# Optimization experiments

Hardware: AMD Instinct MI355X
Metric: run time of the kernel (lower is better)

The kernel has to match this reference:

```python
import jax, jax.numpy as jnp
import numpy as np

G, NPG = 100, 500
N = G * NPG            # 50000 nodes, contiguous equal-size graphs
IN, H = 128, 256
L = 3                  # num_layers
K = 3                  # knn k (loop=True -> self included)
E = 16 * N             # 800000 edges

def setup_inputs():
    key = jax.random.key(0)
    k = jax.random.split(key, 8)
    x = jax.random.normal(k[0], (N, IN), jnp.float32)
    batch = jnp.repeat(jnp.arange(G, dtype=jnp.int32), NPG)
    gid = jax.random.randint(k[1], (E,), 0, G)
    src = jax.random.randint(k[2], (E,), 0, NPG) + gid * NPG
    dst = jax.random.randint(k[3], (E,), 0, NPG) + gid * NPG
    edge_index = jnp.stack([src, dst]).astype(jnp.int32)
    def lin(kk, fin, fout):
        return (jax.random.normal(kk, (fin, fout), jnp.float32) / np.sqrt(fin)).astype(jnp.float32)
    inp = dict(x=x, edge_index=edge_index, batch=batch)
    inp["emb_W"] = lin(k[4], IN, H); inp["emb_b"] = jnp.zeros((H,), jnp.float32)
    inp["conv_W"] = jnp.stack([lin(jax.random.fold_in(k[5], i), H, H) for i in range(L)])
    inp["conv_b"] = jnp.zeros((L, H), jnp.float32)
    inp["fconv_W"] = jnp.stack([lin(jax.random.fold_in(k[6], i), H, H) for i in range(L)])
    inp["fconv_b"] = jnp.zeros((L, H), jnp.float32)
    inp["norm_w"] = jnp.ones((L, H), jnp.float32); inp["norm_b"] = jnp.zeros((L, H), jnp.float32); inp["norm_ms"] = jnp.ones((L, H), jnp.float32)
    inp["fnorm_w"] = jnp.ones((L, H), jnp.float32); inp["fnorm_b"] = jnp.zeros((L, H), jnp.float32); inp["fnorm_ms"] = jnp.ones((L, H), jnp.float32)
    inp["gate_W"] = lin(k[7], 2 * H, H); inp["gate_b"] = jnp.zeros((H,), jnp.float32)
    return inp

def _gcn_conv(h, src, dst, W, b):
    # GCNConv: add self loops, symmetric deg^-1/2 normalization
    m = h @ W                                     # [N,H]
    loop = jnp.arange(N, dtype=src.dtype)
    s2 = jnp.concatenate([src, loop]); d2 = jnp.concatenate([dst, loop])
    deg = jax.ops.segment_sum(jnp.ones_like(d2, jnp.float32), d2, num_segments=N)
    dinv = jnp.where(deg > 0, jax.lax.rsqrt(deg), 0.0)
    coef = (dinv[s2] * dinv[d2])[:, None]
    return jax.ops.segment_sum(m[s2] * coef, d2, num_segments=N) + b

def _graph_norm(x, batch, w, b, ms, cnt):
    # PyG GraphNorm: out = w * (x - ms*mean) / sqrt(var + eps) + b, per-graph stats
    mean = jax.ops.segment_sum(x, batch, num_segments=G) / cnt
    out = x - mean[batch] * ms
    var = jax.ops.segment_sum(out * out, batch, num_segments=G) / cnt
    return w * out * jax.lax.rsqrt(var + 1e-5)[batch] + b

def _knn_graph(x):
    # per-graph cosine knn, loop=True (self has sim 1 and is kept)
    xr = x.reshape(G, NPG, -1)
    xn = xr / (jnp.linalg.norm(xr, axis=-1, keepdims=True) + 1e-12)
    sim = jnp.einsum('gnh,gmh->gnm', xn, xn)      # [G,NPG,NPG]
    _, idx = jax.lax.top_k(sim, K)                # [G,NPG,K]
    offs = (jnp.arange(G) * NPG)[:, None, None]
    src = (idx + offs).reshape(-1)
    dst = jnp.broadcast_to(jnp.arange(N).reshape(G, NPG, 1), (G, NPG, K)).reshape(-1)
    return src.astype(jnp.int32), dst.astype(jnp.int32)

def reference(x, edge_index, batch, emb_W, emb_b, conv_W, conv_b, norm_w, norm_b, norm_ms, fconv_W, fconv_b, fnorm_w, fnorm_b, fnorm_ms, gate_W, gate_b):
    cnt = jax.ops.segment_sum(jnp.ones((N,), jnp.float32), batch, num_segments=G)[:, None]
    h = x @ emb_W + emb_b
    fsrc, fdst = _knn_graph(h)
    src, dst = edge_index[0], edge_index[1]
    all_x = []
    for i in range(L - 1):   # eval mode: dropout is identity
        prev = h
        h = _gcn_conv(h, src, dst, conv_W[i], conv_b[i])
        h = jax.nn.leaky_relu(_graph_norm(h, batch, norm_w[i], norm_b[i], norm_ms[i], cnt))
        f = _gcn_conv(h, fsrc, fdst, fconv_W[i], fconv_b[i])
        f = jax.nn.leaky_relu(_graph_norm(f, batch, fnorm_w[i], fnorm_b[i], fnorm_ms[i], cnt))
        gate = jax.nn.sigmoid(jnp.concatenate([h, f], axis=-1) @ gate_W + gate_b)
        h = gate * h + (1.0 - gate) * f + prev
        all_x.append(h)
    # faithful to source: for i in range(L): += pool(all_x[i-1])  (Python negative indexing!)
    gf = jnp.zeros((G, H), jnp.float32)
    for i in range(L):
        gf = gf + jax.ops.segment_sum(all_x[i - 1], batch, num_segments=G) / cnt
    return gf
```

## Files before the change

kernel.cpp:

```cpp
#include <hip/hip_runtime.h>
#include <math.h>

#define NN 50000
#define GG 100
#define NPGc 500
#define HH 256
#define IND 128

typedef __attribute__((ext_vector_type(8))) short short8v;
typedef __attribute__((ext_vector_type(4))) float f32x4;

__device__ __forceinline__ ushort f2bf(float f) {
    union { float f; unsigned u; } v; v.f = f;
    unsigned r = (v.u + 0x7fffu + ((v.u >> 16) & 1u)) >> 16;
    return (ushort)r;
}
__device__ __forceinline__ float bf2f(ushort h) {
    union { unsigned u; float f; } v; v.u = ((unsigned)h) << 16;
    return v.f;
}

__device__ __forceinline__ int swz(int row, int kidx) { return kidx ^ ((row & 7) << 3); }

__global__ void wcvt(const float* __restrict__ src, ushort* __restrict__ dst, int K, int N)
{
    int i = blockIdx.x * 256 + threadIdx.x;
    if (i < K * N) {
        int n = i / K, k = i % K;
        dst[i] = f2bf(src[(size_t)k * N + n]);
    }
}

__global__ __launch_bounds__(256)
void gemm_mfma(const float* __restrict__ A, const float* __restrict__ A2,
               const ushort* __restrict__ Wt, const float* __restrict__ bias,
               float* __restrict__ C, ushort* __restrict__ Cbf,
               int M, int K, int lda, int mode,
               const float* __restrict__ hn, const float* __restrict__ fn,
               const float* __restrict__ prev)
{
    __shared__ ushort As[128][64];
    __shared__ ushort Bs[128][64];
    const int tid = threadIdx.x;
    const int lane = tid & 63;
    const int w = tid >> 6;
    const int wr = (w >> 1) * 64, wc = (w & 1) * 64;
    const int row0 = blockIdx.x * 128, col0 = blockIdx.y * 128;
    const int lr = lane & 15, lk = (lane >> 4) * 8;
    f32x4 acc[4][4] = {};

    for (int k0 = 0; k0 < K; k0 += 64) {
        __syncthreads();
        #pragma unroll
        for (int it = 0; it < 4; ++it) {
            int c = it * 256 + tid;
            int row = c >> 3, col = (c & 7) * 8;
            int gr = row0 + row; if (gr > M - 1) gr = M - 1;
            const float* Ap = A; int kk = k0 + col;
            if (A2 != nullptr && kk >= 256) { Ap = A2; kk -= 256; }
            const float* s = &Ap[(size_t)gr * lda + kk];
            float4 v0 = *(const float4*)s;
            float4 v1 = *(const float4*)(s + 4);
            union { ushort u[8]; int4 q; } pk;
            pk.u[0] = f2bf(v0.x); pk.u[1] = f2bf(v0.y); pk.u[2] = f2bf(v0.z); pk.u[3] = f2bf(v0.w);
            pk.u[4] = f2bf(v1.x); pk.u[5] = f2bf(v1.y); pk.u[6] = f2bf(v1.z); pk.u[7] = f2bf(v1.w);
            *(int4*)&As[row][swz(row, col)] = pk.q;
        }
        #pragma unroll
        for (int it = 0; it < 4; ++it) {
            int c = it * 256 + tid;
            int n = c >> 3, k = (c & 7) * 8;
            *(int4*)&Bs[n][swz(n, k)] = *(const int4*)&Wt[(size_t)(col0 + n) * K + k0 + k];
        }
        __syncthreads();
        #pragma unroll
        for (int ks = 0; ks < 2; ++ks) {
            short8v av[4], bv[4];
            #pragma unroll
            for (int m = 0; m < 4; ++m) {
                int rr = wr + m * 16 + lr;
                av[m] = *(const short8v*)&As[rr][swz(rr, ks * 32 + lk)];
            }
            #pragma unroll
            for (int n = 0; n < 4; ++n) {
                int rr = wc + n * 16 + lr;
                bv[n] = *(const short8v*)&Bs[rr][swz(rr, ks * 32 + lk)];
            }
            #pragma unroll
            for (int m = 0; m < 4; ++m)
                #pragma unroll
                for (int n = 0; n < 4; ++n)
                    acc[m][n] = __builtin_amdgcn_mfma_f32_16x16x32_bf16(av[m], bv[n], acc[m][n], 0, 0, 0);
        }
    }
    const int fr = (lane >> 4) * 4;
    if (mode == 0) {
        #pragma unroll
        for (int n = 0; n < 4; ++n) {
            int col = col0 + wc + n * 16 + lr;
            float bb = bias ? bias[col] : 0.f;
            #pragma unroll
            for (int m = 0; m < 4; ++m) {
                int rbase = row0 + wr + m * 16 + fr;
                #pragma unroll
                for (int r = 0; r < 4; ++r) {
                    int row = rbase + r;
                    if (row < M) C[(size_t)row * HH + col] = acc[m][n][r] + bb;
                }
            }
        }
    } else if (mode == 2) {
        #pragma unroll
        for (int n = 0; n < 4; ++n) {
            int col = col0 + wc + n * 16 + lr;
            float bb = bias ? bias[col] : 0.f;
            #pragma unroll
            for (int m = 0; m < 4; ++m) {
                int rbase = row0 + wr + m * 16 + fr;
                #pragma unroll
                for (int r = 0; r < 4; ++r) {
                    int row = rbase + r;
                    if (row < M) Cbf[(size_t)row * HH + col] = f2bf(acc[m][n][r] + bb);
                }
            }
        }
    } else {
        #pragma unroll
        for (int n = 0; n < 4; ++n) {
            int col = col0 + wc + n * 16 + lr;
            float gb = bias[col];
            #pragma unroll
            for (int m = 0; m < 4; ++m) {
                int rbase = row0 + wr + m * 16 + fr;
                #pragma unroll
                for (int r = 0; r < 4; ++r) {
                    int row = rbase + r;
                    if (row < M) {
                        size_t o = (size_t)row * HH + col;
                        float z = acc[m][n][r] + gb;
                        float s = 1.f / (1.f + expf(-z));
                        C[o] = s * hn[o] + (1.f - s) * fn[o] + prev[o];
                    }
                }
            }
        }
    }
}

__global__ __launch_bounds__(256)
void row_norm_hl(const float* __restrict__ h, ushort* __restrict__ xh, ushort* __restrict__ xl)
{
    int n = blockIdx.x, c = threadIdx.x;
    float v = h[(size_t)n * HH + c];
    __shared__ float red[256];
    red[c] = v * v;
    __syncthreads();
    for (int s = 128; s > 0; s >>= 1) {
        if (c < s) red[c] += red[c + s];
        __syncthreads();
    }
    float norm = sqrtf(red[0]);
    float xn = v / (norm + 1e-12f);
    ushort hi = f2bf(xn);
    xh[(size_t)n * HH + c] = hi;
    xl[(size_t)n * HH + c] = f2bf(xn - bf2f(hi));
}

__device__ __forceinline__ bool tk_better(float va, int ia, float vb, int ib)
{
    return (va > vb) || (va == vb && ia < ib);
}

__device__ __forceinline__ void ins3(float v, int i,
                                     float& a0, int& b0, float& a1, int& b1,
                                     float& a2, int& b2)
{
    if (tk_better(v, i, a0, b0))      { a2 = a1; b2 = b1; a1 = a0; b1 = b0; a0 = v; b0 = i; }
    else if (tk_better(v, i, a1, b1)) { a2 = a1; b2 = b1; a1 = v;  b1 = i; }
    else if (tk_better(v, i, a2, b2)) { a2 = v;  b2 = i; }
}

__device__ __forceinline__ void merge3(float& v0, float& v1, float& v2,
                                       int& i0, int& i1, int& i2, int off)
{
    float w0 = __shfl_xor(v0, off), w1 = __shfl_xor(v1, off), w2 = __shfl_xor(v2, off);
    int   j0 = __shfl_xor(i0, off), j1 = __shfl_xor(i1, off), j2 = __shfl_xor(i2, off);
    float avv[3] = { v0, v1, v2 }, bvv[3] = { w0, w1, w2 };
    int   aii[3] = { i0, i1, i2 }, bii[3] = { j0, j1, j2 };
    float rv[3]; int ri[3];
    int p = 0, q = 0;
    #pragma unroll
    for (int t = 0; t < 3; ++t) {
        bool takeA = tk_better(avv[p], aii[p], bvv[q], bii[q]);
        rv[t] = takeA ? avv[p] : bvv[q];
        ri[t] = takeA ? aii[p] : bii[q];
        if (takeA) ++p; else ++q;
    }
    v0 = rv[0]; v1 = rv[1]; v2 = rv[2];
    i0 = ri[0]; i1 = ri[1]; i2 = ri[2];
}

__global__ __launch_bounds__(256, 2)
void simtopk(const ushort* __restrict__ xnh, const ushort* __restrict__ xnl,
             int* __restrict__ fsrc)
{
    __shared__ ushort Ash[64][64], Asl[64][64];
    __shared__ ushort Bsh[128][64], Bsl[128][64];
    const int bid = blockIdx.x;
    const int xcd = bid & 7;
    const int rb  = (bid >> 3) & 7;
    const int g   = (bid >> 6) * 8 + xcd;
    if (g >= GG) return;
    const int row0 = rb * 64;
    const int tid  = threadIdx.x;
    const int lane = tid & 63;
    const int w    = tid >> 6;
    const int lr   = lane & 15;
    const int hi4  = lane >> 4;
    const int lk   = hi4 * 8;
    const size_t base = (size_t)g * NPGc * HH;

    float tv0[4], tv1[4], tv2[4];
    int   ti0[4], ti1[4], ti2[4];
    #pragma unroll
    for (int r = 0; r < 4; ++r) {
        tv0[r] = tv1[r] = tv2[r] = -2.f;
        ti0[r] = ti1[r] = ti2[r] = 0x7fffffff;
    }

    for (int ct = 0; ct < 4; ++ct) {
        const int col0 = ct * 128;
        f32x4 acc[8] = {};
        for (int k0 = 0; k0 < HH; k0 += 64) {
            __syncthreads();
            #pragma unroll
            for (int it = 0; it < 2; ++it) {
                int flat = it * 256 + tid;
                int row = flat >> 3, col = (flat & 7) * 8;
                int grow = row0 + row; if (grow > NPGc - 1) grow = NPGc - 1;
                size_t o = base + (size_t)grow * HH + k0 + col;
                *(int4*)&Ash[row][swz(row, col)] = *(const int4*)(xnh + o);
                *(int4*)&Asl[row][swz(row, col)] = *(const int4*)(xnl + o);
            }
            #pragma unroll
            for (int it = 0; it < 4; ++it) {
                int flat = it * 256 + tid;
                int row = flat >> 3, col = (flat & 7) * 8;
                int gcol = col0 + row; if (gcol > NPGc - 1) gcol = NPGc - 1;
                size_t o = base + (size_t)gcol * HH + k0 + col;
                *(int4*)&Bsh[row][swz(row, col)] = *(const int4*)(xnh + o);
                *(int4*)&Bsl[row][swz(row, col)] = *(const int4*)(xnl + o);
            }
            __syncthreads();
            #pragma unroll
            for (int ks = 0; ks < 2; ++ks) {
                const int ra = w * 16 + lr;
                short8v ah = *(const short8v*)&Ash[ra][swz(ra, ks * 32 + lk)];
                short8v al = *(const short8v*)&Asl[ra][swz(ra, ks * 32 + lk)];
                #pragma unroll
                for (int n = 0; n < 8; ++n) {
                    const int rbn = n * 16 + lr;
                    short8v bh = *(const short8v*)&Bsh[rbn][swz(rbn, ks * 32 + lk)];
                    short8v bl = *(const short8v*)&Bsl[rbn][swz(rbn, ks * 32 + lk)];
                    acc[n] = __builtin_amdgcn_mfma_f32_16x16x32_bf16(ah, bh, acc[n], 0, 0, 0);
                    acc[n] = __builtin_amdgcn_mfma_f32_16x16x32_bf16(ah, bl, acc[n], 0, 0, 0);
                    acc[n] = __builtin_amdgcn_mfma_f32_16x16x32_bf16(al, bh, acc[n], 0, 0, 0);
                }
            }
        }
        #pragma unroll
        for (int r = 0; r < 4; ++r) {
            float a0 = tv0[r], a1 = tv1[r], a2 = tv2[r];
            int   b0 = ti0[r], b1 = ti1[r], b2 = ti2[r];
            #pragma unroll
            for (int n = 0; n < 8; ++n) {
                int col = col0 + n * 16 + lr;
                if (col < NPGc)
                    ins3(acc[n][r], col, a0, b0, a1, b1, a2, b2);
            }
            tv0[r] = a0; tv1[r] = a1; tv2[r] = a2;
            ti0[r] = b0; ti1[r] = b1; ti2[r] = b2;
        }
    }

    #pragma unroll
    for (int r = 0; r < 4; ++r) {
        float a0 = tv0[r], a1 = tv1[r], a2 = tv2[r];
        int   b0 = ti0[r], b1 = ti1[r], b2 = ti2[r];
        #pragma unroll
        for (int off = 1; off <= 8; off <<= 1)
            merge3(a0, a1, a2, b0, b1, b2, off);
        if (lr == 0) {
            int row = row0 + w * 16 + hi4 * 4 + r;
            if (row < NPGc) {
                int rg = g * NPGc + row;
                fsrc[rg * 3 + 0] = g * NPGc + b0;
                fsrc[rg * 3 + 1] = g * NPGc + b1;
                fsrc[rg * 3 + 2] = g * NPGc + b2;
            }
        }
    }
}

__global__ void hist_kernel(const int* __restrict__ dst, int* __restrict__ cnt, int nE)
{
    int e = blockIdx.x * 256 + threadIdx.x;
    if (e < nE) atomicAdd(&cnt[dst[e]], 1);
}

__global__ void scan1_kernel(const int* __restrict__ in, int* __restrict__ out,
                             int* __restrict__ bsum, int n)
{
    __shared__ int sh[256];
    int t = threadIdx.x;
    int i = blockIdx.x * 256 + t;
    int v = (i < n) ? in[i] : 0;
    sh[t] = v;
    __syncthreads();
    for (int s = 1; s < 256; s <<= 1) {
        int tv = (t >= s) ? sh[t - s] : 0;
        __syncthreads();
        sh[t] += tv;
        __syncthreads();
    }
    if (i < n) out[i] = sh[t] - v;
    if (t == 255) bsum[blockIdx.x] = sh[255];
}

__global__ void scan2_kernel(int* __restrict__ bsum, int nb)
{
    __shared__ int sh[256];
    int t = threadIdx.x;
    int v = (t < nb) ? bsum[t] : 0;
    sh[t] = v;
    __syncthreads();
    for (int s = 1; s < 256; s <<= 1) {
        int tv = (t >= s) ? sh[t - s] : 0;
        __syncthreads();
        sh[t] += tv;
        __syncthreads();
    }
    if (t < nb) bsum[t] = sh[t] - v;
}

__global__ void scan3_kernel(int* __restrict__ out, const int* __restrict__ bsum, int n)
{
    int i = blockIdx.x * 256 + threadIdx.x;
    if (i < n) out[i] += bsum[blockIdx.x];
}

__global__ void fill_kernel(const int* __restrict__ src, const int* __restrict__ dst,
                            const int* __restrict__ row_ptr, int* __restrict__ cursor,
                            int* __restrict__ sorted_src, int nE)
{
    int e = blockIdx.x * 256 + threadIdx.x;
    if (e < nE) {
        int d = dst[e];
        int pos = row_ptr[d] + atomicAdd(&cursor[d], 1);
        sorted_src[pos] = src[e];
    }
}

__global__ void dinv_kernel(const int* __restrict__ cnt, float* __restrict__ dinv, int n)
{
    int i = blockIdx.x * 256 + threadIdx.x;
    if (i < n) dinv[i] = rsqrtf((float)cnt[i] + 1.0f);
}

__global__ __launch_bounds__(256)
void gcn_gather(const ushort* __restrict__ m, const int* __restrict__ row_ptr,
                const int* __restrict__ cnt, const int* __restrict__ srcs,
                const float* __restrict__ dinv, const float* __restrict__ bias,
                float* __restrict__ out)
{
    int bid = blockIdx.x;
    int xcd = bid & 7, idx = bid >> 3;
    int g = xcd + 8 * (idx / NPGc);
    if (g >= GG) return;
    int n = g * NPGc + (idx % NPGc);
    int c = threadIdx.x;
    float dn = dinv[n];
    float acc = bf2f(m[(size_t)n * HH + c]) * dn;
    int s0 = row_ptr[n], e0 = s0 + cnt[n];
    for (int e = s0; e < e0; ++e) {
        int s = srcs[e];
        acc += bf2f(m[(size_t)s * HH + c]) * dinv[s];
    }
    out[(size_t)n * HH + c] = acc * dn + bias[c];
}

__global__ __launch_bounds__(256)
void fgcn_gather(const ushort* __restrict__ m, const int* __restrict__ fsrc,
                 const float* __restrict__ bias, float* __restrict__ out)
{
    int bid = blockIdx.x;
    int xcd = bid & 7, idx = bid >> 3;
    int g = xcd + 8 * (idx / NPGc);
    if (g >= GG) return;
    int n = g * NPGc + (idx % NPGc);
    int c = threadIdx.x;
    int s0 = fsrc[n * 3], s1 = fsrc[n * 3 + 1], s2 = fsrc[n * 3 + 2];
    float acc = bf2f(m[(size_t)n * HH + c]) + bf2f(m[(size_t)s0 * HH + c])
              + bf2f(m[(size_t)s1 * HH + c]) + bf2f(m[(size_t)s2 * HH + c]);
    out[(size_t)n * HH + c] = 0.25f * acc + bias[c];
}

__global__ __launch_bounds__(256)
void norm_stats(const float* __restrict__ x, float* __restrict__ S1, float* __restrict__ S2)
{
    int g = blockIdx.x, chunk = blockIdx.y, c = threadIdx.x;
    int r0 = chunk * 63, r1 = min(r0 + 63, NPGc);
    float s1 = 0.f, s2 = 0.f;
    for (int r = r0; r < r1; ++r) {
        float v = x[((size_t)(g * NPGc + r)) * HH + c];
        s1 += v; s2 += v * v;
    }
    atomicAdd(&S1[g * HH + c], s1);
    atomicAdd(&S2[g * HH + c], s2);
}

__global__ __launch_bounds__(256)
void norm_apply(float* __restrict__ x, const float* __restrict__ S1, const float* __restrict__ S2,
                const float* __restrict__ w, const float* __restrict__ b,
                const float* __restrict__ ms)
{
    int n = blockIdx.x, c = threadIdx.x;
    int g = n / NPGc;
    size_t o = (size_t)n * HH + c;
    float v = x[o];
    float mean = S1[g * HH + c] / (float)NPGc;
    float mm = mean * ms[c];
    float var = S2[g * HH + c] / (float)NPGc - 2.f * mm * mean + mm * mm;
    float outv = w[c] * (v - mm) * rsqrtf(var + 1e-5f) + b[c];
    x[o] = outv > 0.f ? outv : 0.01f * outv;
}

__global__ __launch_bounds__(256)
void pool_kernel(const float* __restrict__ X0, const float* __restrict__ X1,
                 float* __restrict__ out)
{
    int g = blockIdx.x, c = threadIdx.x;
    float s0 = 0.f, s1 = 0.f;
    for (int r = 0; r < NPGc; ++r) {
        size_t o = ((size_t)(g * NPGc + r)) * HH + c;
        s0 += X0[o];
        s1 += X1[o];
    }
    out[g * HH + c] = (s0 + 2.f * s1) / (float)NPGc;
}

__global__ void sentinel_kernel(float* out, int n)
{
    int i = blockIdx.x * 256 + threadIdx.x;
    if (i < n) out[i] = 12345.0f;
}

extern "C" void kernel_launch(void* const* d_in, const int* in_sizes, int n_in,
                              void* d_out, int out_size, void* d_ws, size_t ws_size,
                              hipStream_t stream)
{
    const float* x       = (const float*)d_in[0];
    const int* edge_idx  = (const int*)d_in[1];
    const float* emb_W   = (const float*)d_in[3];
    const float* emb_b   = (const float*)d_in[4];
    const float* conv_W  = (const float*)d_in[5];
    const float* conv_b  = (const float*)d_in[6];
    const float* fconv_W = (const float*)d_in[7];
    const float* fconv_b = (const float*)d_in[8];
    const float* norm_w  = (const float*)d_in[9];
    const float* norm_b  = (const float*)d_in[10];
    const float* norm_ms = (const float*)d_in[11];
    const float* fnorm_w = (const float*)d_in[12];
    const float* fnorm_b = (const float*)d_in[13];
    const float* fnorm_ms= (const float*)d_in[14];
    const float* gate_W  = (const float*)d_in[15];
    const float* gate_b  = (const float*)d_in[16];

    const int E = in_sizes[1] / 2;
    const int* esrc = edge_idx;
    const int* edst = edge_idx + E;

    const size_t NHf = (size_t)NN * HH;
    char* p = (char*)d_ws;
    auto alloc = [&](size_t bytes) { char* r = p; p += (bytes + 255) & ~(size_t)255; return r; };
    float* B0 = (float*)alloc(NHf * 4);
    float* B1 = (float*)alloc(NHf * 4);
    float* B2 = (float*)alloc(NHf * 4);
    float* B3 = (float*)alloc(NHf * 4);
    ushort* xnh = (ushort*)B2;
    ushort* xnl = xnh + NHf;
    ushort* msgbf = (ushort*)alloc(NHf * 2);
    int* sorted_src = (int*)alloc((size_t)E * 4);
    int* row_ptr    = (int*)alloc((size_t)NN * 4);
    int* deg_cnt    = (int*)alloc((size_t)NN * 4);
    int* cursor     = (int*)alloc((size_t)NN * 4);
    float* dinv     = (float*)alloc((size_t)NN * 4);
    int* fsrc       = (int*)alloc((size_t)NN * 3 * 4);
    float* S1       = (float*)alloc((size_t)GG * HH * 4);
    float* S2       = (float*)alloc((size_t)GG * HH * 4);
    int* bsum       = (int*)alloc(1024);
    ushort* wts     = (ushort*)alloc((size_t)425984 * 2);
    size_t needed = (size_t)(p - (char*)d_ws);
    if (ws_size < needed) {
        sentinel_kernel<<<(out_size + 255) / 256, 256, 0, stream>>>((float*)d_out, out_size);
        return;
    }
    ushort* embWt   = wts;
    ushort* convWt0 = wts + 32768;
    ushort* convWt1 = wts + 32768 + 65536;
    ushort* fconvWt0 = wts + 163840;
    ushort* fconvWt1 = wts + 163840 + 65536;
    ushort* gateWt  = wts + 294912;

    const int nScanB = (NN + 255) / 256;
    const int gatherGrid = 8 * 13 * NPGc;

    hipMemsetAsync(deg_cnt, 0, (size_t)NN * 4, stream);
    hipMemsetAsync(cursor, 0, (size_t)NN * 4, stream);

    wcvt<<<(32768 + 255) / 256, 256, 0, stream>>>(emb_W, embWt, IND, HH);
    wcvt<<<(65536 + 255) / 256, 256, 0, stream>>>(conv_W, convWt0, HH, HH);
    wcvt<<<(65536 + 255) / 256, 256, 0, stream>>>(conv_W + 65536, convWt1, HH, HH);
    wcvt<<<(65536 + 255) / 256, 256, 0, stream>>>(fconv_W, fconvWt0, HH, HH);
    wcvt<<<(65536 + 255) / 256, 256, 0, stream>>>(fconv_W + 65536, fconvWt1, HH, HH);
    wcvt<<<(131072 + 255) / 256, 256, 0, stream>>>(gate_W, gateWt, 2 * HH, HH);

    dim3 ggrid((NN + 127) / 128, 2);
    gemm_mfma<<<ggrid, 256, 0, stream>>>(x, nullptr, embWt, emb_b, B0, nullptr,
                                         NN, IND, IND, 0, nullptr, nullptr, nullptr);

    hist_kernel<<<(E + 255) / 256, 256, 0, stream>>>(edst, deg_cnt, E);
    scan1_kernel<<<nScanB, 256, 0, stream>>>(deg_cnt, row_ptr, bsum, NN);
    scan2_kernel<<<1, 256, 0, stream>>>(bsum, nScanB);
    scan3_kernel<<<nScanB, 256, 0, stream>>>(row_ptr, bsum, NN);
    fill_kernel<<<(E + 255) / 256, 256, 0, stream>>>(esrc, edst, row_ptr, cursor, sorted_src, E);
    dinv_kernel<<<(NN + 255) / 256, 256, 0, stream>>>(deg_cnt, dinv, NN);

    row_norm_hl<<<NN, 256, 0, stream>>>(B0, xnh, xnl);
    simtopk<<<832, 256, 0, stream>>>(xnh, xnl, fsrc);

    float* h  = B0;
    float* mb = B1;
    dim3 ngrid(GG, 8);
    for (int i = 0; i < 2; ++i) {
        const ushort* Wc = (i == 0) ? convWt0 : convWt1;
        const ushort* Wf = (i == 0) ? fconvWt0 : fconvWt1;
        const float* bc  = conv_b  + (size_t)i * HH;
        const float* bf  = fconv_b + (size_t)i * HH;
        gemm_mfma<<<ggrid, 256, 0, stream>>>(h, nullptr, Wc, nullptr, nullptr, msgbf,
                                             NN, HH, HH, 2, nullptr, nullptr, nullptr);
        gcn_gather<<<gatherGrid, 256, 0, stream>>>(msgbf, row_ptr, deg_cnt, sorted_src,
                                                   dinv, bc, B2);
        hipMemsetAsync(S1, 0, (size_t)2 * GG * HH * 4, stream);
        norm_stats<<<ngrid, 256, 0, stream>>>(B2, S1, S2);
        norm_apply<<<NN, 256, 0, stream>>>(B2, S1, S2, norm_w + i * HH, norm_b + i * HH,
                                           norm_ms + i * HH);
        gemm_mfma<<<ggrid, 256, 0, stream>>>(B2, nullptr, Wf, nullptr, nullptr, msgbf,
                                             NN, HH, HH, 2, nullptr, nullptr, nullptr);
        fgcn_gather<<<gatherGrid, 256, 0, stream>>>(msgbf, fsrc, bf, B3);
        hipMemsetAsync(S1, 0, (size_t)2 * GG * HH * 4, stream);
        norm_stats<<<ngrid, 256, 0, stream>>>(B3, S1, S2);
        norm_apply<<<NN, 256, 0, stream>>>(B3, S1, S2, fnorm_w + i * HH, fnorm_b + i * HH,
                                           fnorm_ms + i * HH);
        gemm_mfma<<<ggrid, 256, 0, stream>>>(B2, B3, gateWt, gate_b, mb, nullptr,
                                             NN, 2 * HH, HH, 1, B2, B3, h);
        float* t = h; h = mb; mb = t;
    }
    pool_kernel<<<GG, 256, 0, stream>>>(mb, h, (float*)d_out);
}
```

Measured before the change: 1.322 ms.

## Use direct global-to-LDS loads with pre-swizzled layouts and drop stats atomics

Weight and normalized-feature buffers are now written in global memory already XOR-swizzled, so GEMM and similarity kernels can stream tiles straight into LDS with global_load_lds instead of going through registers. The simtopk launch-bounds occupancy hint is removed. Graph-norm statistics are written as per-chunk partials that norm_apply sums itself, which removes the atomics and the per-layer memsets. This adds reads of eight partials per element in norm_apply, and the LDS layout assumed by the direct loads has to match the swizzle exactly.

```diff
diff --git a/kernel.cpp b/kernel.cpp
--- a/kernel.cpp
+++ b/kernel.cpp
@@ -22,12 +22,19 @@
 
 __device__ __forceinline__ int swz(int row, int kidx) { return kidx ^ ((row & 7) << 3); }
 
+__device__ __forceinline__ void llds16(const ushort* g, ushort* l)
+{
+    __builtin_amdgcn_global_load_lds(
+        (const __attribute__((address_space(1))) void*)g,
+        (__attribute__((address_space(3))) void*)l, 16, 0, 0);
+}
+
 __global__ void wcvt(const float* __restrict__ src, ushort* __restrict__ dst, int K, int N)
 {
     int i = blockIdx.x * 256 + threadIdx.x;
     if (i < K * N) {
         int n = i / K, k = i % K;
-        dst[i] = f2bf(src[(size_t)k * N + n]);
+        dst[(size_t)n * K + (k ^ ((n & 7) << 3))] = f2bf(src[(size_t)k * N + n]);
     }
 }
 
@@ -67,10 +74,12 @@
             *(int4*)&As[row][swz(row, col)] = pk.q;
         }
         #pragma unroll
-        for (int it = 0; it < 4; ++it) {
-            int c = it * 256 + tid;
-            int n = c >> 3, k = (c & 7) * 8;
-            *(int4*)&Bs[n][swz(n, k)] = *(const int4*)&Wt[(size_t)(col0 + n) * K + k0 + k];
+        for (int i = 0; i < 4; ++i) {
+            int ch = w * 4 + i;
+            int brow = ch * 8 + (lane >> 3);
+            int gq = lane & 7;
+            llds16(&Wt[(size_t)(col0 + brow) * K + k0 + gq * 8],
+                   &Bs[0][0] + ch * 512);
         }
         __syncthreads();
         #pragma unroll
@@ -162,8 +171,9 @@
     float norm = sqrtf(red[0]);
     float xn = v / (norm + 1e-12f);
     ushort hi = f2bf(xn);
-    xh[(size_t)n * HH + c] = hi;
-    xl[(size_t)n * HH + c] = f2bf(xn - bf2f(hi));
+    int cs = c ^ ((n & 7) << 3);
+    xh[(size_t)n * HH + cs] = hi;
+    xl[(size_t)n * HH + cs] = f2bf(xn - bf2f(hi));
 }
 
 __device__ __forceinline__ bool tk_better(float va, int ia, float vb, int ib)
@@ -200,12 +210,12 @@
     i0 = ri[0]; i1 = ri[1]; i2 = ri[2];
 }
 
-__global__ __launch_bounds__(256, 2)
+__global__ __launch_bounds__(256)
 void simtopk(const ushort* __restrict__ xnh, const ushort* __restrict__ xnl,
              int* __restrict__ fsrc)
 {
-    __shared__ ushort Ash[64][64], Asl[64][64];
-    __shared__ ushort Bsh[128][64], Bsl[128][64];
+    __shared__ ushort AshL[64][64], AslL[64][64];
+    __shared__ ushort BshL[128][64], BslL[128][64];
     const int bid = blockIdx.x;
     const int xcd = bid & 7;
     const int rb  = (bid >> 3) & 7;
@@ -219,6 +229,7 @@
     const int hi4  = lane >> 4;
     const int lk   = hi4 * 8;
     const size_t base = (size_t)g * NPGc * HH;
+    const int r8 = lane >> 3, gq = lane & 7;
 
     float tv0[4], tv1[4], tv2[4];
     int   ti0[4], ti1[4], ti2[4];
@@ -234,34 +245,41 @@
         for (int k0 = 0; k0 < HH; k0 += 64) {
             __syncthreads();
             #pragma unroll
-            for (int it = 0; it < 2; ++it) {
-                int flat = it * 256 + tid;
-                int row = flat >> 3, col = (flat & 7) * 8;
-                int grow = row0 + row; if (grow > NPGc - 1) grow = NPGc - 1;
-                size_t o = base + (size_t)grow * HH + k0 + col;
-                *(int4*)&Ash[row][swz(row, col)] = *(const int4*)(xnh + o);
-                *(int4*)&Asl[row][swz(row, col)] = *(const int4*)(xnl + o);
-            }
-            #pragma unroll
-            for (int it = 0; it < 4; ++it) {
-                int flat = it * 256 + tid;
-                int row = flat >> 3, col = (flat & 7) * 8;
-                int gcol = col0 + row; if (gcol > NPGc - 1) gcol = NPGc - 1;
-                size_t o = base + (size_t)gcol * HH + k0 + col;
-                *(int4*)&Bsh[row][swz(row, col)] = *(const int4*)(xnh + o);
-                *(int4*)&Bsl[row][swz(row, col)] = *(const int4*)(xnl + o);
+            for (int i = 0; i < 12; ++i) {
+                int ch = w * 12 + i;
+                if (ch < 8) {
+                    int row = ch * 8 + r8;
+                    int gr = row0 + row; if (gr > NPGc - 1) gr = NPGc - 1;
+                    llds16(xnh + base + (size_t)gr * HH + k0 + gq * 8,
+                           &AshL[0][0] + ch * 512);
+                } else if (ch < 16) {
+                    int row = (ch - 8) * 8 + r8;
+                    int gr = row0 + row; if (gr > NPGc - 1) gr = NPGc - 1;
+                    llds16(xnl + base + (size_t)gr * HH + k0 + gq * 8,
+                           &AslL[0][0] + (ch - 8) * 512);
+                } else if (ch < 32) {
+                    int row = (ch - 16) * 8 + r8;
+                    int gc = col0 + row; if (gc > NPGc - 1) gc = NPGc - 1;
+                    llds16(xnh + base + (size_t)gc * HH + k0 + gq * 8,
+                           &BshL[0][0] + (ch - 16) * 512);
+                } else {
+                    int row = (ch - 32) * 8 + r8;
+                    int gc = col0 + row; if (gc > NPGc - 1) gc = NPGc - 1;
+                    llds16(xnl + base + (size_t)gc * HH + k0 + gq * 8,
+                           &BslL[0][0] + (ch - 32) * 512);
+                }
             }
             __syncthreads();
             #pragma unroll
             for (int ks = 0; ks < 2; ++ks) {
                 const int ra = w * 16 + lr;
-                short8v ah = *(const short8v*)&Ash[ra][swz(ra, ks * 32 + lk)];
-                short8v al = *(const short8v*)&Asl[ra][swz(ra, ks * 32 + lk)];
+                short8v ah = *(const short8v*)&AshL[ra][swz(ra, ks * 32 + lk)];
+                short8v al = *(const short8v*)&AslL[ra][swz(ra, ks * 32 + lk)];
                 #pragma unroll
                 for (int n = 0; n < 8; ++n) {
                     const int rbn = n * 16 + lr;
-                    short8v bh = *(const short8v*)&Bsh[rbn][swz(rbn, ks * 32 + lk)];
-                    short8v bl = *(const short8v*)&Bsl[rbn][swz(rbn, ks * 32 + lk)];
+                    short8v bh = *(const short8v*)&BshL[rbn][swz(rbn, ks * 32 + lk)];
+                    short8v bl = *(const short8v*)&BslL[rbn][swz(rbn, ks * 32 + lk)];
                     acc[n] = __builtin_amdgcn_mfma_f32_16x16x32_bf16(ah, bh, acc[n], 0, 0, 0);
                     acc[n] = __builtin_amdgcn_mfma_f32_16x16x32_bf16(ah, bl, acc[n], 0, 0, 0);
                     acc[n] = __builtin_amdgcn_mfma_f32_16x16x32_bf16(al, bh, acc[n], 0, 0, 0);
@@ -406,7 +424,7 @@
 }
 
 __global__ __launch_bounds__(256)
-void norm_stats(const float* __restrict__ x, float* __restrict__ S1, float* __restrict__ S2)
+void norm_stats(const float* __restrict__ x, float* __restrict__ S1p, float* __restrict__ S2p)
 {
     int g = blockIdx.x, chunk = blockIdx.y, c = threadIdx.x;
     int r0 = chunk * 63, r1 = min(r0 + 63, NPGc);
@@ -415,12 +433,13 @@
         float v = x[((size_t)(g * NPGc + r)) * HH + c];
         s1 += v; s2 += v * v;
     }
-    atomicAdd(&S1[g * HH + c], s1);
-    atomicAdd(&S2[g * HH + c], s2);
-}
-
-__global__ __launch_bounds__(256)
-void norm_apply(float* __restrict__ x, const float* __restrict__ S1, const float* __restrict__ S2,
+    size_t o = ((size_t)(g * 8 + chunk)) * HH + c;
+    S1p[o] = s1;
+    S2p[o] = s2;
+}
+
+__global__ __launch_bounds__(256)
+void norm_apply(float* __restrict__ x, const float* __restrict__ S1p, const float* __restrict__ S2p,
                 const float* __restrict__ w, const float* __restrict__ b,
                 const float* __restrict__ ms)
 {
@@ -428,9 +447,16 @@
     int g = n / NPGc;
     size_t o = (size_t)n * HH + c;
     float v = x[o];
-    float mean = S1[g * HH + c] / (float)NPGc;
+    float s1 = 0.f, s2 = 0.f;
+    #pragma unroll
+    for (int j = 0; j < 8; ++j) {
+        size_t po = ((size_t)(g * 8 + j)) * HH + c;
+        s1 += S1p[po];
+        s2 += S2p[po];
+    }
+    float mean = s1 / (float)NPGc;
     float mm = mean * ms[c];
-    float var = S2[g * HH + c] / (float)NPGc - 2.f * mm * mean + mm * mm;
+    float var = s2 / (float)NPGc - 2.f * mm * mean + mm * mm;
     float outv = w[c] * (v - mm) * rsqrtf(var + 1e-5f) + b[c];
     x[o] = outv > 0.f ? outv : 0.01f * outv;
 }
@@ -496,8 +522,8 @@
     int* cursor     = (int*)alloc((size_t)NN * 4);
     float* dinv     = (float*)alloc((size_t)NN * 4);
     int* fsrc       = (int*)alloc((size_t)NN * 3 * 4);
-    float* S1       = (float*)alloc((size_t)GG * HH * 4);
-    float* S2       = (float*)alloc((size_t)GG * HH * 4);
+    float* S1p      = (float*)alloc((size_t)GG * 8 * HH * 4);
+    float* S2p      = (float*)alloc((size_t)GG * 8 * HH * 4);
     int* bsum       = (int*)alloc(1024);
     ushort* wts     = (ushort*)alloc((size_t)425984 * 2);
     size_t needed = (size_t)(p - (char*)d_ws);
@@ -551,16 +577,14 @@
                                              NN, HH, HH, 2, nullptr, nullptr, nullptr);
         gcn_gather<<<gatherGrid, 256, 0, stream>>>(msgbf, row_ptr, deg_cnt, sorted_src,
                                                    dinv, bc, B2);
-        hipMemsetAsync(S1, 0, (size_t)2 * GG * HH * 4, stream);
-        norm_stats<<<ngrid, 256, 0, stream>>>(B2, S1, S2);
-        norm_apply<<<NN, 256, 0, stream>>>(B2, S1, S2, norm_w + i * HH, norm_b + i * HH,
+        norm_stats<<<ngrid, 256, 0, stream>>>(B2, S1p, S2p);
+        norm_apply<<<NN, 256, 0, stream>>>(B2, S1p, S2p, norm_w + i * HH, norm_b + i * HH,
                                            norm_ms + i * HH);
         gemm_mfma<<<ggrid, 256, 0, stream>>>(B2, nullptr, Wf, nullptr, nullptr, msgbf,
                                              NN, HH, HH, 2, nullptr, nullptr, nullptr);
         fgcn_gather<<<gatherGrid, 256, 0, stream>>>(msgbf, fsrc, bf, B3);
-        hipMemsetAsync(S1, 0, (size_t)2 * GG * HH * 4, stream);
-        norm_stats<<<ngrid, 256, 0, stream>>>(B3, S1, S2);
-        norm_apply<<<NN, 256, 0, stream>>>(B3, S1, S2, fnorm_w + i * HH, fnorm_b + i * HH,
+        norm_stats<<<ngrid, 256, 0, stream>>>(B3, S1p, S2p);
+        norm_apply<<<NN, 256, 0, stream>>>(B3, S1p, S2p, fnorm_w + i * HH, fnorm_b + i * HH,
                                            fnorm_ms + i * HH);
         gemm_mfma<<<ggrid, 256, 0, stream>>>(B2, B3, gateWt, gate_b, mb, nullptr,
                                              NN, 2 * HH, HH, 1, B2, B3, h);
```

Result: slower. 1.483 ms (+12.2%).
